# Performance work log

Measured on AMD Instinct MI355X. Metric: run time of the kernel, lower is better.

The kernel has to match this reference:

```python
import jax, jax.numpy as jnp
import numpy as np

TOP_K = 8


def setup_inputs() -> dict:
    key = jax.random.key(0)
    k1, k2 = jax.random.split(key)
    B, L, D = 32, 8192, 256
    x = jax.random.normal(k1, (B, L, D), dtype=jnp.float32)
    # lengths in [TOP_K, L]; mask = 1 where padded (positions >= length)
    lengths = jax.random.randint(k2, (B,), TOP_K, L + 1)
    x_mask = (jnp.arange(L)[None, :] >= lengths[:, None]).astype(jnp.int32)
    return {"x": x, "x_mask": x_mask}


def reference(x, x_mask):
    # Masked top-k over the sequence axis (dim=1), per feature channel.
    # Padded positions (mask==1) are filled with -inf so they are never
    # selected, matching the original's per-row i[:l] slicing (valid-first).
    B, L, D = x.shape
    neg_inf = jnp.finfo(x.dtype).min
    masked = jnp.where(x_mask[:, :, None] > 0, neg_inf, x)  # [B, L, D]
    vals, _ = jax.lax.top_k(jnp.swapaxes(masked, 1, 2), TOP_K)  # [B, D, k]
    out = jnp.swapaxes(vals, 1, 2).reshape(B, TOP_K * D)  # [B, k*D]
    return out
```

## Files before the change

### kernel.cpp

```cpp
#include <hip/hip_runtime.h>
#include <cfloat>


#define TOPK 8
#define BB 32
#define LL 8192
#define DD 256

__device__ __forceinline__ void insert8(float r[TOPK], float v) {
    r[7] = fmaxf(r[7], v);
#pragma unroll
    for (int j = TOPK - 1; j > 0; --j) {
        float hi = fmaxf(r[j - 1], r[j]);
        float lo = fminf(r[j - 1], r[j]);
        r[j - 1] = hi;
        r[j] = lo;
    }
}

__global__ __launch_bounds__(256, 4) void topk_pass1(
    const float* __restrict__ x, const int* __restrict__ mask,
    float* __restrict__ ws, int nchunk, int cl) {
    const int b = blockIdx.x;
    const int chunk = blockIdx.y;
    const int d = threadIdx.x;
    const int l0 = chunk * cl;
    const int* mrow = mask + b * LL;

    const int mfirst = mrow[l0];
    const int mlast = mrow[l0 + cl - 1];

    int nvalid;
    if (mfirst) {
        nvalid = 0;
    } else if (!mlast) {
        nvalid = cl;
    } else {
        int lo = l0 + 1, hi = l0 + cl - 1;
        while (lo < hi) {
            int mid = (lo + hi) >> 1;
            if (mrow[mid]) hi = mid; else lo = mid + 1;
        }
        nvalid = lo - l0;
    }

    float r[TOPK];
#pragma unroll
    for (int k = 0; k < TOPK; ++k) r[k] = -FLT_MAX;

    const float* xp = x + ((size_t)b * LL + l0) * DD + d;
    int l = 0;
    for (; l + 4 <= nvalid; l += 4) {
        float v0 = xp[(size_t)(l + 0) * DD];
        float v1 = xp[(size_t)(l + 1) * DD];
        float v2 = xp[(size_t)(l + 2) * DD];
        float v3 = xp[(size_t)(l + 3) * DD];
        insert8(r, v0);
        insert8(r, v1);
        insert8(r, v2);
        insert8(r, v3);
    }
    for (; l < nvalid; ++l) insert8(r, xp[(size_t)l * DD]);

    float* wp = ws + ((size_t)(b * nchunk + chunk) * TOPK) * DD + d;
#pragma unroll
    for (int k = 0; k < TOPK; ++k) wp[(size_t)k * DD] = r[k];
}

__global__ __launch_bounds__(256, 4) void topk_pass2(
    const float* __restrict__ ws, float* __restrict__ out, int P) {
    __shared__ float lds[4 * TOPK * 64];
    const int b = blockIdx.x;
    const int q = blockIdx.y;
    const int c = threadIdx.x & 63;
    const int ps = threadIdx.x >> 6;
    const int d = q * 64 + c;
    const int lists = P >> 2;

    float r[TOPK];
#pragma unroll
    for (int k = 0; k < TOPK; ++k) r[k] = -FLT_MAX;

    const float* wp = ws + ((size_t)b * P + (size_t)ps * lists) * TOPK * DD + d;
    for (int j = 0; j < lists; ++j) {
#pragma unroll
        for (int k = 0; k < TOPK; ++k) {
            insert8(r, wp[((size_t)j * TOPK + k) * DD]);
        }
    }

#pragma unroll
    for (int k = 0; k < TOPK; ++k) lds[(ps * TOPK + k) * 64 + c] = r[k];
    __syncthreads();

    if (ps == 0) {
#pragma unroll
        for (int p2 = 1; p2 < 4; ++p2) {
#pragma unroll
            for (int k = 0; k < TOPK; ++k) {
                insert8(r, lds[(p2 * TOPK + k) * 64 + c]);
            }
        }
        float* op = out + (size_t)b * (TOPK * DD) + d;
#pragma unroll
        for (int k = 0; k < TOPK; ++k) op[(size_t)k * DD] = r[k];
    }
}

__global__ __launch_bounds__(256) void topk_fallback(
    const float* __restrict__ x, const int* __restrict__ mask,
    float* __restrict__ out) {
    const int b = blockIdx.x;
    const int d = threadIdx.x;
    const int* mrow = mask + b * LL;
    int lo = 0, hi = LL;
    while (lo < hi) {
        int mid = (lo + hi) >> 1;
        if (mrow[mid]) hi = mid; else lo = mid + 1;
    }
    const int len = lo;

    float r[TOPK];
#pragma unroll
    for (int k = 0; k < TOPK; ++k) r[k] = -FLT_MAX;

    const float* xp = x + (size_t)b * LL * DD + d;
    int l = 0;
    for (; l + 4 <= len; l += 4) {
        float v0 = xp[(size_t)(l + 0) * DD];
        float v1 = xp[(size_t)(l + 1) * DD];
        float v2 = xp[(size_t)(l + 2) * DD];
        float v3 = xp[(size_t)(l + 3) * DD];
        insert8(r, v0);
        insert8(r, v1);
        insert8(r, v2);
        insert8(r, v3);
    }
    for (; l < len; ++l) insert8(r, xp[(size_t)l * DD]);

    float* op = out + (size_t)b * (TOPK * DD) + d;
#pragma unroll
    for (int k = 0; k < TOPK; ++k) op[(size_t)k * DD] = r[k];
}

extern "C" void kernel_launch(void* const* d_in, const int* in_sizes, int n_in,
                              void* d_out, int out_size, void* d_ws, size_t ws_size,
                              hipStream_t stream) {
    const float* x = (const float*)d_in[0];
    const int* mask = (const int*)d_in[1];
    float* out = (float*)d_out;

    int nchunk = 32;
    while (nchunk > 2 && (size_t)BB * nchunk * TOPK * DD * 4 > ws_size) nchunk >>= 1;

    if (nchunk >= 4) {
        float* ws = (float*)d_ws;
        dim3 g1(BB, nchunk);
        topk_pass1<<<g1, 256, 0, stream>>>(x, mask, ws, nchunk, LL / nchunk);
        dim3 g2(BB, 4);
        topk_pass2<<<g2, 256, 0, stream>>>(ws, out, nchunk);
    } else {
        topk_fallback<<<BB, 256, 0, stream>>>(x, mask, out);
    }
}
```

Baseline: 345.4 us.

## Use 64-row chunks per wave with float4 loads and length-aware reduction

Pass 1 now gives each wavefront one 64-row chunk. Each lane loads a float4 and keeps four independent top-8 lists, which widens memory accesses and grows the grid to 128 chunks per batch. Fully padded chunks exit early and skip their workspace write. Pass 2 recomputes the valid length from the mask and merges only the chunks that hold valid data, using 8 waves per block. The cost is a larger workspace (needs 128 chunks) and a higher register footprint from four top-8 lists per lane.

Measured after the change: 360.1 us. 4.3% more time.

```diff
diff --git a/kernel.cpp b/kernel.cpp
--- a/kernel.cpp
+++ b/kernel.cpp
@@ -6,104 +6,115 @@
 #define BB 32
 #define LL 8192
 #define DD 256
+#define CL 64
+#define NC (LL / CL)
 
-__device__ __forceinline__ void insert8(float r[TOPK], float v) {
-    r[7] = fmaxf(r[7], v);
-#pragma unroll
-    for (int j = TOPK - 1; j > 0; --j) {
-        float hi = fmaxf(r[j - 1], r[j]);
-        float lo = fminf(r[j - 1], r[j]);
-        r[j - 1] = hi;
-        r[j] = lo;
+struct Top8 { float r0, r1, r2, r3, r4, r5, r6, r7; };
+
+#define CMPX(a, b) { float _hi = fmaxf(a, b); float _lo = fminf(a, b); (a) = _hi; (b) = _lo; }
+
+__device__ __forceinline__ void t8_init(Top8& t) {
+    t.r0 = t.r1 = t.r2 = t.r3 = t.r4 = t.r5 = t.r6 = t.r7 = -FLT_MAX;
+}
+
+__device__ __forceinline__ void t8_ins(Top8& t, float v) {
+    t.r7 = fmaxf(t.r7, v);
+    CMPX(t.r6, t.r7); CMPX(t.r5, t.r6); CMPX(t.r4, t.r5); CMPX(t.r3, t.r4);
+    CMPX(t.r2, t.r3); CMPX(t.r1, t.r2); CMPX(t.r0, t.r1);
+}
+
+__device__ __forceinline__ int mask_lower_bound(const int* mrow, int lo0, int hi0) {
+    int lo = lo0, hi = hi0;
+    while (lo < hi) {
+        int mid = (lo + hi) >> 1;
+        if (mrow[mid]) hi = mid; else lo = mid + 1;
     }
+    return lo;
 }
 
 __global__ __launch_bounds__(256, 4) void topk_pass1(
     const float* __restrict__ x, const int* __restrict__ mask,
-    float* __restrict__ ws, int nchunk, int cl) {
+    float* __restrict__ ws) {
     const int b = blockIdx.x;
-    const int chunk = blockIdx.y;
-    const int d = threadIdx.x;
-    const int l0 = chunk * cl;
+    const int lane = threadIdx.x & 63;
+    const int wv = threadIdx.x >> 6;
+    const int chunk = blockIdx.y * 4 + wv;
+    const int l0 = chunk * CL;
     const int* mrow = mask + b * LL;
 
-    const int mfirst = mrow[l0];
-    const int mlast = mrow[l0 + cl - 1];
+    if (mrow[l0]) return;
 
     int nvalid;
-    if (mfirst) {
-        nvalid = 0;
-    } else if (!mlast) {
-        nvalid = cl;
+    if (!mrow[l0 + CL - 1]) {
+        nvalid = CL;
     } else {
-        int lo = l0 + 1, hi = l0 + cl - 1;
-        while (lo < hi) {
-            int mid = (lo + hi) >> 1;
-            if (mrow[mid]) hi = mid; else lo = mid + 1;
-        }
-        nvalid = lo - l0;
+        nvalid = mask_lower_bound(mrow, l0 + 1, l0 + CL - 1) - l0;
     }
 
-    float r[TOPK];
-#pragma unroll
-    for (int k = 0; k < TOPK; ++k) r[k] = -FLT_MAX;
+    Top8 t0, t1, t2, t3;
+    t8_init(t0); t8_init(t1); t8_init(t2); t8_init(t3);
 
-    const float* xp = x + ((size_t)b * LL + l0) * DD + d;
-    int l = 0;
-    for (; l + 4 <= nvalid; l += 4) {
-        float v0 = xp[(size_t)(l + 0) * DD];
-        float v1 = xp[(size_t)(l + 1) * DD];
-        float v2 = xp[(size_t)(l + 2) * DD];
-        float v3 = xp[(size_t)(l + 3) * DD];
-        insert8(r, v0);
-        insert8(r, v1);
-        insert8(r, v2);
-        insert8(r, v3);
+    const float4* xp = (const float4*)(x + ((size_t)b * LL + l0) * DD) + lane;
+    float4 v = xp[0];
+    for (int l = 1; l < nvalid; ++l) {
+        float4 nv = xp[(size_t)l * (DD / 4)];
+        t8_ins(t0, v.x); t8_ins(t1, v.y); t8_ins(t2, v.z); t8_ins(t3, v.w);
+        v = nv;
     }
-    for (; l < nvalid; ++l) insert8(r, xp[(size_t)l * DD]);
+    t8_ins(t0, v.x); t8_ins(t1, v.y); t8_ins(t2, v.z); t8_ins(t3, v.w);
 
-    float* wp = ws + ((size_t)(b * nchunk + chunk) * TOPK) * DD + d;
-#pragma unroll
-    for (int k = 0; k < TOPK; ++k) wp[(size_t)k * DD] = r[k];
+    float4* wp = (float4*)(ws + ((size_t)(b * NC + chunk) * TOPK) * DD) + lane;
+    wp[0 * (DD / 4)] = make_float4(t0.r0, t1.r0, t2.r0, t3.r0);
+    wp[1 * (DD / 4)] = make_float4(t0.r1, t1.r1, t2.r1, t3.r1);
+    wp[2 * (DD / 4)] = make_float4(t0.r2, t1.r2, t2.r2, t3.r2);
+    wp[3 * (DD / 4)] = make_float4(t0.r3, t1.r3, t2.r3, t3.r3);
+    wp[4 * (DD / 4)] = make_float4(t0.r4, t1.r4, t2.r4, t3.r4);
+    wp[5 * (DD / 4)] = make_float4(t0.r5, t1.r5, t2.r5, t3.r5);
+    wp[6 * (DD / 4)] = make_float4(t0.r6, t1.r6, t2.r6, t3.r6);
+    wp[7 * (DD / 4)] = make_float4(t0.r7, t1.r7, t2.r7, t3.r7);
 }
 
-__global__ __launch_bounds__(256, 4) void topk_pass2(
-    const float* __restrict__ ws, float* __restrict__ out, int P) {
-    __shared__ float lds[4 * TOPK * 64];
+__global__ __launch_bounds__(512) void topk_pass2(
+    const float* __restrict__ ws, const int* __restrict__ mask,
+    float* __restrict__ out) {
+    __shared__ float lds[8 * TOPK * 64];
     const int b = blockIdx.x;
     const int q = blockIdx.y;
     const int c = threadIdx.x & 63;
     const int ps = threadIdx.x >> 6;
     const int d = q * 64 + c;
-    const int lists = P >> 2;
+    const int* mrow = mask + b * LL;
 
-    float r[TOPK];
-#pragma unroll
-    for (int k = 0; k < TOPK; ++k) r[k] = -FLT_MAX;
+    const int len = mask_lower_bound(mrow, 0, LL);
+    const int nvc = (len + CL - 1) / CL;
 
-    const float* wp = ws + ((size_t)b * P + (size_t)ps * lists) * TOPK * DD + d;
-    for (int j = 0; j < lists; ++j) {
-#pragma unroll
-        for (int k = 0; k < TOPK; ++k) {
-            insert8(r, wp[((size_t)j * TOPK + k) * DD]);
-        }
+    Top8 t;
+    t8_init(t);
+    for (int j = ps; j < nvc; j += 8) {
+        const float* wp = ws + ((size_t)(b * NC + j) * TOPK) * DD + d;
+        t8_ins(t, wp[0 * DD]); t8_ins(t, wp[1 * DD]);
+        t8_ins(t, wp[2 * DD]); t8_ins(t, wp[3 * DD]);
+        t8_ins(t, wp[4 * DD]); t8_ins(t, wp[5 * DD]);
+        t8_ins(t, wp[6 * DD]); t8_ins(t, wp[7 * DD]);
     }
 
-#pragma unroll
-    for (int k = 0; k < TOPK; ++k) lds[(ps * TOPK + k) * 64 + c] = r[k];
+    float* lp = lds + ps * TOPK * 64 + c;
+    lp[0 * 64] = t.r0; lp[1 * 64] = t.r1; lp[2 * 64] = t.r2; lp[3 * 64] = t.r3;
+    lp[4 * 64] = t.r4; lp[5 * 64] = t.r5; lp[6 * 64] = t.r6; lp[7 * 64] = t.r7;
     __syncthreads();
 
     if (ps == 0) {
 #pragma unroll
-        for (int p2 = 1; p2 < 4; ++p2) {
-#pragma unroll
-            for (int k = 0; k < TOPK; ++k) {
-                insert8(r, lds[(p2 * TOPK + k) * 64 + c]);
-            }
+        for (int p = 1; p < 8; ++p) {
+            const float* rp = lds + p * TOPK * 64 + c;
+            t8_ins(t, rp[0 * 64]); t8_ins(t, rp[1 * 64]);
+            t8_ins(t, rp[2 * 64]); t8_ins(t, rp[3 * 64]);
+            t8_ins(t, rp[4 * 64]); t8_ins(t, rp[5 * 64]);
+            t8_ins(t, rp[6 * 64]); t8_ins(t, rp[7 * 64]);
         }
         float* op = out + (size_t)b * (TOPK * DD) + d;
-#pragma unroll
-        for (int k = 0; k < TOPK; ++k) op[(size_t)k * DD] = r[k];
+        op[0 * DD] = t.r0; op[1 * DD] = t.r1; op[2 * DD] = t.r2; op[3 * DD] = t.r3;
+        op[4 * DD] = t.r4; op[5 * DD] = t.r5; op[6 * DD] = t.r6; op[7 * DD] = t.r7;
     }
 }
 
@@ -113,34 +124,16 @@
     const int b = blockIdx.x;
     const int d = threadIdx.x;
     const int* mrow = mask + b * LL;
-    int lo = 0, hi = LL;
-    while (lo < hi) {
-        int mid = (lo + hi) >> 1;
-        if (mrow[mid]) hi = mid; else lo = mid + 1;
-    }
-    const int len = lo;
+    const int len = mask_lower_bound(mrow, 0, LL);
 
-    float r[TOPK];
-#pragma unroll
-    for (int k = 0; k < TOPK; ++k) r[k] = -FLT_MAX;
-
+    Top8 t;
+    t8_init(t);
     const float* xp = x + (size_t)b * LL * DD + d;
-    int l = 0;
-    for (; l + 4 <= len; l += 4) {
-        float v0 = xp[(size_t)(l + 0) * DD];
-        float v1 = xp[(size_t)(l + 1) * DD];
-        float v2 = xp[(size_t)(l + 2) * DD];
-        float v3 = xp[(size_t)(l + 3) * DD];
-        insert8(r, v0);
-        insert8(r, v1);
-        insert8(r, v2);
-        insert8(r, v3);
-    }
-    for (; l < len; ++l) insert8(r, xp[(size_t)l * DD]);
+    for (int l = 0; l < len; ++l) t8_ins(t, xp[(size_t)l * DD]);
 
     float* op = out + (size_t)b * (TOPK * DD) + d;
-#pragma unroll
-    for (int k = 0; k < TOPK; ++k) op[(size_t)k * DD] = r[k];
+    op[0 * DD] = t.r0; op[1 * DD] = t.r1; op[2 * DD] = t.r2; op[3 * DD] = t.r3;
+    op[4 * DD] = t.r4; op[5 * DD] = t.r5; op[6 * DD] = t.r6; op[7 * DD] = t.r7;
 }
 
 extern "C" void kernel_launch(void* const* d_in, const int* in_sizes, int n_in,
@@ -150,15 +143,13 @@
     const int* mask = (const int*)d_in[1];
     float* out = (float*)d_out;
 
-    int nchunk = 32;
-    while (nchunk > 2 && (size_t)BB * nchunk * TOPK * DD * 4 > ws_size) nchunk >>= 1;
-
-    if (nchunk >= 4) {
+    const size_t ws_need = (size_t)BB * NC * TOPK * DD * 4;
+    if (ws_size >= ws_need) {
         float* ws = (float*)d_ws;
-        dim3 g1(BB, nchunk);
-        topk_pass1<<<g1, 256, 0, stream>>>(x, mask, ws, nchunk, LL / nchunk);
+        dim3 g1(BB, NC / 4);
+        topk_pass1<<<g1, 256, 0, stream>>>(x, mask, ws);
         dim3 g2(BB, 4);
-        topk_pass2<<<g2, 256, 0, stream>>>(ws, out, nchunk);
+        topk_pass2<<<g2, 512, 0, stream>>>(ws, mask, out);
     } else {
         topk_fallback<<<BB, 256, 0, stream>>>(x, mask, out);
     }
```
